# Kernel tuning notes

Hardware: AMD Instinct MI355X
Metric: run time of the kernel (lower is better)

Reference implementation:

```python
import math
import jax, jax.numpy as jnp
import numpy as np

D_MODEL, N_STATE, SEQ_LEN = 1024, 64, 1024
DT_MIN, DT_MAX = 1e-3, 1e-1


def setup_inputs() -> dict:
    key = jax.random.key(0)
    kC, kdt = jax.random.split(key)
    A_real = -0.5 * jnp.ones((D_MODEL, N_STATE), jnp.float32)
    A_imag = math.pi * jnp.broadcast_to(
        jnp.arange(N_STATE, dtype=jnp.float32), (D_MODEL, N_STATE)
    )
    C = jax.random.normal(kC, (D_MODEL, N_STATE, 2), jnp.float32) * 0.5
    log_dt = (
        jax.random.uniform(kdt, (D_MODEL,), jnp.float32)
        * (math.log(DT_MAX) - math.log(DT_MIN))
        + math.log(DT_MIN)
    )
    B = jnp.ones((D_MODEL, N_STATE), jnp.float32)
    return {"A_real": A_real, "A_imag": A_imag, "C": C, "log_dt": log_dt,
            "B": B, "L": SEQ_LEN}


def reference(A_real, A_imag, C, log_dt, B, L):
    dt = jnp.exp(log_dt)                       # (d,)
    A = A_real + 1j * A_imag                   # (d,N) complex64
    dtA = A * dt[:, None]                      # (d,N)
    Cc = C[..., 0] + 1j * C[..., 1]            # (d,N) complex64
    ell = jnp.arange(L, dtype=jnp.float32)     # (L,)
    # A_bar ** l == exp(dtA * l): Vandermonde power expansion, (d,N,L)
    powers = jnp.exp(dtA[..., None] * ell)
    K = jnp.einsum('dn,dnl->dl', Cc * B.astype(Cc.dtype), powers)  # (d,L)
    return K.real * dt[:, None]
```

## Files before the change

kernel.cpp:

```cpp
#include <hip/hip_runtime.h>
#include <math.h>


#define D_MODEL 1024
#define N_STATE 64
#define SEQ_LEN 1024
#define CHUNK   8
#define TPD     128
#define NSPLIT  2
#define NPT     (N_STATE / NSPLIT)
#define BLOCK   (TPD * NSPLIT)

#define INV_2PI 0.15915494309189535

__device__ __forceinline__ float sin_rev(float f) { return __builtin_amdgcn_sinf(f); }
__device__ __forceinline__ float cos_rev(float f) { return __builtin_amdgcn_cosf(f); }

__global__ __launch_bounds__(BLOCK, 4) void s4d_kernel(
    const float* __restrict__ A_real, const float* __restrict__ A_imag,
    const float* __restrict__ C, const float* __restrict__ log_dt,
    const float* __restrict__ B, float* __restrict__ out)
{
  __shared__ float2 hiT[N_STATE][8];
  __shared__ float2 loT[N_STATE][16];
  __shared__ float4 ws[N_STATE];
  __shared__ float  red[CHUNK][TPD];

  const int tid = threadIdx.x;
  const int d   = blockIdx.x;
  const float dt = __expf(log_dt[d]);

  #pragma unroll
  for (int i = 0; i < 6; ++i) {
    const int e   = tid + BLOCK * i;
    const int n   = e / 24;
    const int idx = e - n * 24;
    const int steps = (idx < 8) ? (idx << 4) : (idx - 8);
    const float ar = A_real[d * N_STATE + n];
    const float ai = A_imag[d * N_STATE + n];
    const float xr = dt * ar;
    const double drev = (double)dt * (double)ai * INV_2PI;
    const double ph = drev * (double)steps;
    const float  fr = (float)(ph - floor(ph));
    const float mag = __expf(xr * (float)steps);
    const float2 v = make_float2(mag * cos_rev(fr), mag * sin_rev(fr));
    if (idx < 8) hiT[n][idx] = v; else loT[n][idx - 8] = v;
  }
  if (tid < N_STATE) {
    const int n = tid;
    const float ar = A_real[d * N_STATE + n];
    const float ai = A_imag[d * N_STATE + n];
    const float b  = B[d * N_STATE + n];
    const float cr = C[(d * N_STATE + n) * 2 + 0];
    const float ci = C[(d * N_STATE + n) * 2 + 1];
    const float xr = dt * ar;
    const double drev = (double)dt * (double)ai * INV_2PI;
    const double ph = drev * 128.0;
    const float  fr = (float)(ph - floor(ph));
    const float mag = __expf(xr * 128.0f);
    ws[n] = make_float4(cr * b * dt, ci * b * dt,
                        mag * cos_rev(fr), mag * sin_rev(fr));
  }
  __syncthreads();

  const int t     = tid & (TPD - 1);
  const int split = tid >> 7;
  const int thi   = t >> 4;
  const int tlo   = t & 15;

  float acc[CHUNK];
  #pragma unroll
  for (int j = 0; j < CHUNK; ++j) acc[j] = 0.0f;

  const int n0 = split * NPT;
  #pragma unroll 4
  for (int nn = 0; nn < NPT; ++nn) {
    const int n = n0 + nn;
    const float4 w4 = ws[n];
    const float2 h  = hiT[n][thi];
    const float2 l2 = loT[n][tlo];
    const float sr = fmaf(h.x, l2.x, -(h.y * l2.y));
    const float si = fmaf(h.x, l2.y,   h.y * l2.x);
    float u0 = fmaf(w4.x, sr, -(w4.y * si));
    const float yi = fmaf(w4.x, si, w4.y * sr);
    float u1 = fmaf(u0, w4.z, -(yi * w4.w));
    const float a2 = w4.z + w4.z;
    const float nb = -fmaf(w4.z, w4.z, w4.w * w4.w);
    acc[0] += u0;
    acc[1] += u1;
    #pragma unroll
    for (int j = 2; j < CHUNK; ++j) {
      const float u2 = fmaf(a2, u1, nb * u0);
      acc[j] += u2;
      u0 = u1; u1 = u2;
    }
  }

  if (split == 1) {
    #pragma unroll
    for (int j = 0; j < CHUNK; ++j) red[j][t] = acc[j];
  }
  __syncthreads();
  if (split == 0) {
    float* op = out + d * SEQ_LEN + t;
    #pragma unroll
    for (int j = 0; j < CHUNK; ++j) op[j * TPD] = acc[j] + red[j][t];
  }
}

extern "C" void kernel_launch(void* const* d_in, const int* in_sizes, int n_in,
                              void* d_out, int out_size, void* d_ws, size_t ws_size,
                              hipStream_t stream) {
  const float* A_real = (const float*)d_in[0];
  const float* A_imag = (const float*)d_in[1];
  const float* C      = (const float*)d_in[2];
  const float* log_dt = (const float*)d_in[3];
  const float* B      = (const float*)d_in[4];
  float* out = (float*)d_out;

  s4d_kernel<<<dim3(D_MODEL), dim3(BLOCK), 0, stream>>>(
      A_real, A_imag, C, log_dt, B, out);
}
```

Before: 72.67 us.

## Split state dimension four ways and fold C weights into high-step table

Doubles the number of state-splits per block, giving 512 threads that each handle 16 states, and reduces all four partial sums through shared memory with a cooperative store. The C·B·dt weight is multiplied into the high-step power table during setup. The recurrence coefficients are also precomputed into shared memory, which takes several multiplies out of the inner loop. This raises per-block parallelism and trims per-iteration arithmetic, at the cost of a larger shared reduction buffer and an extra reduction pass.

```diff
diff --git a/kernel.cpp b/kernel.cpp
--- a/kernel.cpp
+++ b/kernel.cpp
@@ -7,7 +7,7 @@
 #define SEQ_LEN 1024
 #define CHUNK   8
 #define TPD     128
-#define NSPLIT  2
+#define NSPLIT  4
 #define NPT     (N_STATE / NSPLIT)
 #define BLOCK   (TPD * NSPLIT)
 
@@ -16,22 +16,22 @@
 __device__ __forceinline__ float sin_rev(float f) { return __builtin_amdgcn_sinf(f); }
 __device__ __forceinline__ float cos_rev(float f) { return __builtin_amdgcn_cosf(f); }
 
-__global__ __launch_bounds__(BLOCK, 4) void s4d_kernel(
+__global__ __launch_bounds__(BLOCK, 8) void s4d_kernel(
     const float* __restrict__ A_real, const float* __restrict__ A_imag,
     const float* __restrict__ C, const float* __restrict__ log_dt,
     const float* __restrict__ B, float* __restrict__ out)
 {
-  __shared__ float2 hiT[N_STATE][8];
+  __shared__ float2 whT[N_STATE][8];
   __shared__ float2 loT[N_STATE][16];
   __shared__ float4 ws[N_STATE];
-  __shared__ float  red[CHUNK][TPD];
+  __shared__ float  red[NSPLIT][CHUNK][TPD];
 
   const int tid = threadIdx.x;
   const int d   = blockIdx.x;
   const float dt = __expf(log_dt[d]);
 
   #pragma unroll
-  for (int i = 0; i < 6; ++i) {
+  for (int i = 0; i < 3; ++i) {
     const int e   = tid + BLOCK * i;
     const int n   = e / 24;
     const int idx = e - n * 24;
@@ -43,23 +43,30 @@
     const double ph = drev * (double)steps;
     const float  fr = (float)(ph - floor(ph));
     const float mag = __expf(xr * (float)steps);
-    const float2 v = make_float2(mag * cos_rev(fr), mag * sin_rev(fr));
-    if (idx < 8) hiT[n][idx] = v; else loT[n][idx - 8] = v;
+    const float vr = mag * cos_rev(fr);
+    const float vi = mag * sin_rev(fr);
+    if (idx < 8) {
+      const float b  = B[d * N_STATE + n];
+      const float cr = C[(d * N_STATE + n) * 2 + 0] * b * dt;
+      const float ci = C[(d * N_STATE + n) * 2 + 1] * b * dt;
+      whT[n][idx] = make_float2(fmaf(cr, vr, -(ci * vi)),
+                                fmaf(cr, vi,   ci * vr));
+    } else {
+      loT[n][idx - 8] = make_float2(vr, vi);
+    }
   }
   if (tid < N_STATE) {
     const int n = tid;
     const float ar = A_real[d * N_STATE + n];
     const float ai = A_imag[d * N_STATE + n];
-    const float b  = B[d * N_STATE + n];
-    const float cr = C[(d * N_STATE + n) * 2 + 0];
-    const float ci = C[(d * N_STATE + n) * 2 + 1];
     const float xr = dt * ar;
     const double drev = (double)dt * (double)ai * INV_2PI;
     const double ph = drev * 128.0;
     const float  fr = (float)(ph - floor(ph));
     const float mag = __expf(xr * 128.0f);
-    ws[n] = make_float4(cr * b * dt, ci * b * dt,
-                        mag * cos_rev(fr), mag * sin_rev(fr));
+    const float str = mag * cos_rev(fr);
+    const float sti = mag * sin_rev(fr);
+    ws[n] = make_float4(str, sti, str + str, -fmaf(str, str, sti * sti));
   }
   __syncthreads();
 
@@ -73,38 +80,36 @@
   for (int j = 0; j < CHUNK; ++j) acc[j] = 0.0f;
 
   const int n0 = split * NPT;
-  #pragma unroll 4
+  #pragma unroll 2
   for (int nn = 0; nn < NPT; ++nn) {
     const int n = n0 + nn;
     const float4 w4 = ws[n];
-    const float2 h  = hiT[n][thi];
-    const float2 l2 = loT[n][tlo];
-    const float sr = fmaf(h.x, l2.x, -(h.y * l2.y));
-    const float si = fmaf(h.x, l2.y,   h.y * l2.x);
-    float u0 = fmaf(w4.x, sr, -(w4.y * si));
-    const float yi = fmaf(w4.x, si, w4.y * sr);
-    float u1 = fmaf(u0, w4.z, -(yi * w4.w));
-    const float a2 = w4.z + w4.z;
-    const float nb = -fmaf(w4.z, w4.z, w4.w * w4.w);
+    const float2 wh = whT[n][thi];
+    const float2 lo = loT[n][tlo];
+    float u0       = fmaf(wh.x, lo.x, -(wh.y * lo.y));
+    const float yi = fmaf(wh.x, lo.y,   wh.y * lo.x);
+    float u1 = fmaf(u0, w4.x, -(yi * w4.y));
     acc[0] += u0;
     acc[1] += u1;
     #pragma unroll
     for (int j = 2; j < CHUNK; ++j) {
-      const float u2 = fmaf(a2, u1, nb * u0);
+      const float u2 = fmaf(w4.z, u1, w4.w * u0);
       acc[j] += u2;
       u0 = u1; u1 = u2;
     }
   }
 
-  if (split == 1) {
-    #pragma unroll
-    for (int j = 0; j < CHUNK; ++j) red[j][t] = acc[j];
-  }
+  #pragma unroll
+  for (int j = 0; j < CHUNK; ++j) red[split][j][t] = acc[j];
   __syncthreads();
-  if (split == 0) {
-    float* op = out + d * SEQ_LEN + t;
-    #pragma unroll
-    for (int j = 0; j < CHUNK; ++j) op[j * TPD] = acc[j] + red[j][t];
+
+  #pragma unroll
+  for (int i = 0; i < 2; ++i) {
+    const int e  = tid + BLOCK * i;
+    const int j  = e >> 7;
+    const int tt = e & 127;
+    out[d * SEQ_LEN + j * TPD + tt] =
+        red[0][j][tt] + red[1][j][tt] + red[2][j][tt] + red[3][j][tt];
   }
 }
 
```

After: 72.08 us. About the same (-0.8%).
